# Optimization experiments

Measured on AMD Instinct MI355X. Metric: run time of the kernel, lower is better.

The kernel has to match this reference:

```python
import jax, jax.numpy as jnp
import numpy as np

N = 100000   # nodes
E = 1600000  # edges (nnz of sparse A)
H = 128      # hidden_size


def _row_normalize(x):
    # F.normalize(x, p=1, dim=1): divide each row by max(L1 norm, 1e-12); zero-out infs
    norm = jnp.sum(jnp.abs(x), axis=1, keepdims=True)
    y = x / jnp.maximum(norm, 1e-12)
    return jnp.where(jnp.isinf(y), 0.0, y)


def setup_inputs() -> dict:
    key = jax.random.key(0)
    k = jax.random.split(key, 7)
    x = jax.random.normal(k[0], (N, H), dtype=jnp.float32)
    A_rows = jax.random.randint(k[1], (E,), 0, N, dtype=jnp.int32)
    A_cols = jax.random.randint(k[2], (E,), 0, N, dtype=jnp.int32)
    A_vals = jax.random.uniform(k[3], (E,), dtype=jnp.float32)
    W = jax.random.normal(k[4], (H, H), dtype=jnp.float32) / np.float32(np.sqrt(H))
    b = jax.random.normal(k[5], (H,), dtype=jnp.float32) * 0.01
    time_step = jax.random.uniform(k[6], (1,), dtype=jnp.float32)
    return {"x": x, "A_rows": A_rows, "A_cols": A_cols, "A_vals": A_vals,
            "W": W, "b": b, "time_step": time_step}


def reference(x, A_rows, A_cols, A_vals, W, b, time_step):
    shortcut = x
    xn = _row_normalize(x)                       # normalize=True
    # sparse.mm(A, x): gather neighbor rows, scale by edge value, scatter-add to dst rows
    msgs = A_vals[:, None] * xn[A_cols]          # [E, H]
    f = jax.ops.segment_sum(msgs, A_rows, num_segments=N)  # [N, H]
    f = f @ W.T + b                              # time_varying=True linear
    # dropout p=0 -> identity (eval semantics)
    f = _row_normalize(f)                        # normalize=True
    f = jnp.maximum(f, 0.0)                      # relu
    return shortcut + f * time_step[0]           # Euler residual with learned step
```

## Files before the change

kernel.cpp:

```cpp
#include <hip/hip_runtime.h>

constexpr int HD = 128;
constexpr int BROWS = 64;
constexpr int CAP = 2048;
constexpr int NBMAX = 2048;
constexpr int EPB = 16384;
constexpr int SLOT_STRIDE = 4096;
constexpr int SLOT_BYTES = 32768;

typedef __attribute__((ext_vector_type(8))) short short8v;
typedef __attribute__((ext_vector_type(4))) float f32x4;
typedef __attribute__((ext_vector_type(2))) float f32x2;

__device__ __forceinline__ int rl(int v, int j) {
    return __builtin_amdgcn_readlane(v, j);
}
__device__ __forceinline__ float rlf(int v, int j) {
    return __uint_as_float((unsigned)__builtin_amdgcn_readlane(v, j));
}
__device__ __forceinline__ unsigned f2bf(float f) {
    unsigned u = __float_as_uint(f);
    return (u + 0x7fffu + ((u >> 16) & 1u)) >> 16;
}
__device__ __forceinline__ f32x2 bf2f(unsigned u) {
    f32x2 r = {__uint_as_float(u << 16), __uint_as_float(u & 0xffff0000u)};
    return r;
}

#define META_OFF_MASK 0x03FFFF00

__global__ void init_kernel(int* __restrict__ cursor, int NB) {
    int i = blockIdx.x * 1024 + threadIdx.x;
    if (i < NB) cursor[i] = 0;
}

__global__ void __launch_bounds__(512) build_kernel(
    const float* __restrict__ x, unsigned* __restrict__ xb,
    float* __restrict__ xnorm, const float* __restrict__ W,
    unsigned* __restrict__ Wb, const int* __restrict__ rows,
    const int* __restrict__ cols, const float* __restrict__ vals,
    int* __restrict__ cursor, int2* __restrict__ outslots,
    int2* __restrict__ lastslot, int N, int E, int PB, int NB) {
    int bid = blockIdx.x;
    int tid = threadIdx.x;
    if (bid < PB) {
        int row = bid * 8 + (tid >> 6);
        int lane = tid & 63;
        if (row >= N) return;
        float2 v = *((const float2*)(x + (size_t)row * HD) + lane);
        float s = fabsf(v.x) + fabsf(v.y);
#pragma unroll
        for (int m = 1; m < 64; m <<= 1) s += __shfl_xor(s, m, 64);
        float nm = fmaxf(s, 1e-12f);
        float rn = 1.0f / nm;
        if (lane == 0) xnorm[row] = nm;
        unsigned lo = f2bf(v.x * rn), hi = f2bf(v.y * rn);
        xb[(size_t)row * 64 + lane] = lo | (hi << 16);
    } else if (bid < PB + 16) {
        int t = (bid - PB) * 512 + tid;
        int col = t >> 6, k2 = t & 63;
        float w0 = W[col * HD + 2 * k2];
        float w1 = W[col * HD + 2 * k2 + 1];
        unsigned pk = f2bf(w0) | (f2bf(w1) << 16);
        int byte = (col * 256 + k2 * 4) ^ ((col & 7) << 4);
        *(unsigned*)((char*)Wb + byte) = pk;
    } else {
        int sb = bid - PB - 16;
        if (NB <= NBMAX) {
            __shared__ int lbin[NBMAX];
            __shared__ int lbase[NBMAX];
            __shared__ unsigned short rk16[EPB];
            for (int i = tid; i < NBMAX; i += 512) lbin[i] = 0;
            __syncthreads();
            const int4* rows4 = (const int4*)rows;
            int E4 = E >> 2;
            int base4 = sb * (EPB / 4);
#pragma unroll
            for (int i = 0; i < 8; ++i) {
                int e4 = base4 + i * 512 + tid;
                if (e4 < E4) {
                    int4 r = rows4[e4];
                    int li = (i * 512 + tid) * 4;
                    rk16[li + 0] = (unsigned short)atomicAdd(&lbin[r.x >> 6], 1);
                    rk16[li + 1] = (unsigned short)atomicAdd(&lbin[r.y >> 6], 1);
                    rk16[li + 2] = (unsigned short)atomicAdd(&lbin[r.z >> 6], 1);
                    rk16[li + 3] = (unsigned short)atomicAdd(&lbin[r.w >> 6], 1);
                }
            }
            __syncthreads();
            for (int i = tid; i < NB; i += 512) {
                int c = lbin[i];
                if (c) lbase[i] = atomicAdd(&cursor[i], c);
            }
            __syncthreads();
            const int4* cols4 = (const int4*)cols;
            const float4* vals4 = (const float4*)vals;
#pragma unroll
            for (int i = 0; i < 8; ++i) {
                int e4 = base4 + i * 512 + tid;
                if (e4 < E4) {
                    int4 r4 = rows4[e4];
                    int4 c4 = cols4[e4];
                    float4 v4 = vals4[e4];
                    int li = (i * 512 + tid) * 4;
                    int ra[4] = {r4.x, r4.y, r4.z, r4.w};
                    int ca[4] = {c4.x, c4.y, c4.z, c4.w};
                    float va[4] = {v4.x, v4.y, v4.z, v4.w};
#pragma unroll
                    for (int k = 0; k < 4; ++k) {
                        int r = ra[k];
                        int bkt = r >> 6;
                        int idx = lbase[bkt] + rk16[li + k];
                        if (idx < CAP) {
                            int2* sp = (bkt == NB - 1)
                                           ? lastslot
                                           : outslots + (size_t)bkt * SLOT_STRIDE;
                            sp[idx] = make_int2((ca[k] << 8) | ((r & 63) << 26),
                                                __float_as_int(va[k]));
                        }
                    }
                }
            }
            if (sb == 0) {
                for (int e = (E & ~3) + tid; e < E; e += 512) {
                    int r = rows[e];
                    int bkt = r >> 6;
                    int rel = atomicAdd(&cursor[bkt], 1);
                    if (rel < CAP) {
                        int2* sp = (bkt == NB - 1)
                                       ? lastslot
                                       : outslots + (size_t)bkt * SLOT_STRIDE;
                        sp[rel] = make_int2((cols[e] << 8) | ((r & 63) << 26),
                                            __float_as_int(vals[e]));
                    }
                }
            }
        } else {
            int base = sb * EPB;
            for (int i = 0; i < 32; ++i) {
                int e = base + i * 512 + tid;
                if (e >= E) break;
                int r = rows[e];
                int bkt = r >> 6;
                int rel = atomicAdd(&cursor[bkt], 1);
                if (rel < CAP) {
                    int2* sp = (bkt == NB - 1)
                                   ? lastslot
                                   : outslots + (size_t)bkt * SLOT_STRIDE;
                    sp[rel] = make_int2((cols[e] << 8) | ((r & 63) << 26),
                                        __float_as_int(vals[e]));
                }
            }
        }
    }
}

__global__ void __launch_bounds__(1024) mega_kernel(
    const unsigned* __restrict__ xb, const float* __restrict__ xnorm,
    const int* __restrict__ cursor, const int2* __restrict__ lastslot,
    const unsigned* __restrict__ Wb, const float* __restrict__ bias,
    const float* __restrict__ tsp, float* out, int N, int NB) {
    __shared__ char wb_raw[HD * HD * 2];
    __shared__ char fb_raw[BROWS * HD * 2];
    __shared__ int2 sorted[CAP];
    __shared__ int lcnt[BROWS], lbeg[BROWS], lcur[BROWS];
    __shared__ float rowsum[BROWS];

    int tid = threadIdx.x;
    int bid = blockIdx.x;
    const int2* slot = (bid == NB - 1)
                           ? lastslot
                           : (const int2*)((const char*)out +
                                           (size_t)bid * SLOT_BYTES);
    int ct = cursor[bid];
    if (ct > CAP) ct = CAP;

    if (tid < BROWS) lcnt[tid] = 0;

    int2 m0 = make_int2(0, 0), m1 = make_int2(0, 0);
    bool e0 = tid < ct, e1 = tid + 1024 < ct;
    if (e0) m0 = slot[tid];
    if (e1) m1 = slot[tid + 1024];
    __syncthreads();

    if (e0) atomicAdd(&lcnt[(unsigned)m0.x >> 26], 1);
    if (e1) atomicAdd(&lcnt[(unsigned)m1.x >> 26], 1);
    __syncthreads();

    if (tid < 64) {
        int c = lcnt[tid];
        int s = c;
#pragma unroll
        for (int m = 1; m < 64; m <<= 1) {
            int t2 = __shfl_up(s, m, 64);
            if (tid >= m) s += t2;
        }
        lbeg[tid] = s - c;
        lcur[tid] = s - c;
    }
    __syncthreads();

    if (e0) {
        int p = atomicAdd(&lcur[(unsigned)m0.x >> 26], 1);
        if (p < CAP) sorted[p] = m0;
    }
    if (e1) {
        int p = atomicAdd(&lcur[(unsigned)m1.x >> 26], 1);
        if (p < CAP) sorted[p] = m1;
    }
    {
        const float4* s4 = (const float4*)Wb;
        float4* d4 = (float4*)wb_raw;
        for (int i = tid; i < HD * HD * 2 / 16; i += 1024) d4[i] = s4[i];
    }
    __syncthreads();

    int lane = tid & 63;
    int wid = tid >> 6;
    float ts = tsp[0];
    const char* xbl = (const char*)xb + (lane << 2);

    float a0[4], a1[4];
#pragma unroll
    for (int rr = 0; rr < 4; ++rr) {
        int lr = wid * 4 + rr;
        int beg = lbeg[lr], cnt = lcnt[lr];
        f32x2 pq0 = {0.f, 0.f}, pq1 = {0.f, 0.f};
        for (int jb = 0; jb < cnt; jb += 64) {
            int rem = cnt - jb;
            if (rem > 64) rem = 64;
            int2 meta = make_int2(0, 0);
            if (lane < rem) meta = sorted[beg + jb + lane];
            int j = 0;
            for (; j + 4 <= rem; j += 4) {
                int o0 = rl(meta.x, j) & META_OFF_MASK;
                int o1 = rl(meta.x, j + 1) & META_OFF_MASK;
                int o2 = rl(meta.x, j + 2) & META_OFF_MASK;
                int o3 = rl(meta.x, j + 3) & META_OFF_MASK;
                float s0 = rlf(meta.y, j), s1 = rlf(meta.y, j + 1);
                float s2 = rlf(meta.y, j + 2), s3 = rlf(meta.y, j + 3);
                unsigned u0 = *(const unsigned*)(xbl + o0);
                unsigned u1 = *(const unsigned*)(xbl + o1);
                unsigned u2 = *(const unsigned*)(xbl + o2);
                unsigned u3 = *(const unsigned*)(xbl + o3);
                pq0 += bf2f(u0) * s0;
                pq1 += bf2f(u1) * s1;
                pq0 += bf2f(u2) * s2;
                pq1 += bf2f(u3) * s3;
            }
            for (; j < rem; ++j) {
                int o0 = rl(meta.x, j) & META_OFF_MASK;
                float s0 = rlf(meta.y, j);
                unsigned u0 = *(const unsigned*)(xbl + o0);
                pq0 += bf2f(u0) * s0;
            }
        }
        a0[rr] = pq0.x + pq1.x;
        a1[rr] = pq0.y + pq1.y;
    }

#pragma unroll
    for (int rr = 0; rr < 4; ++rr) {
        int row = wid * 4 + rr;
        unsigned pk = f2bf(a0[rr]) | (f2bf(a1[rr]) << 16);
        int byte = (row * 256 + lane * 4) ^ ((row & 7) << 4);
        *(unsigned*)(fb_raw + byte) = pk;
    }
    if (tid < BROWS) rowsum[tid] = 0.f;
    __syncthreads();

    int rt = wid >> 2;
    int ct0 = (wid & 3) * 2;
    int c = lane & 15;
    int kg = lane >> 4;
    int arow = rt * 16 + c;
    int bcol0 = ct0 * 16 + c;
    int bcol1 = bcol0 + 16;
    f32x4 acc0 = {0.f, 0.f, 0.f, 0.f}, acc1 = {0.f, 0.f, 0.f, 0.f};
#pragma unroll
    for (int kk = 0; kk < 4; ++kk) {
        int ka = kg * 16 + kk * 64;
        short8v af = *(const short8v*)(fb_raw +
                                       ((arow * 256 + ka) ^ ((arow & 7) << 4)));
        short8v bf0 = *(const short8v*)(wb_raw +
                                        ((bcol0 * 256 + ka) ^ ((bcol0 & 7) << 4)));
        short8v bf1 = *(const short8v*)(wb_raw +
                                        ((bcol1 * 256 + ka) ^ ((bcol1 & 7) << 4)));
        acc0 = __builtin_amdgcn_mfma_f32_16x16x32_bf16(af, bf0, acc0, 0, 0, 0);
        acc1 = __builtin_amdgcn_mfma_f32_16x16x32_bf16(af, bf1, acc1, 0, 0, 0);
    }

    float bias0 = bias[bcol0];
    float bias1 = bias[bcol1];
    float g0r[4], g1r[4];
#pragma unroll
    for (int r = 0; r < 4; ++r) {
        float v0 = acc0[r] + bias0;
        float v1 = acc1[r] + bias1;
        g0r[r] = v0;
        g1r[r] = v1;
        float s = fabsf(v0) + fabsf(v1);
        s += __shfl_xor(s, 1, 64);
        s += __shfl_xor(s, 2, 64);
        s += __shfl_xor(s, 4, 64);
        s += __shfl_xor(s, 8, 64);
        if (c == 0) atomicAdd(&rowsum[rt * 16 + kg * 4 + r], s);
    }
    __syncthreads();
#pragma unroll
    for (int r = 0; r < 4; ++r) {
        int lrow = rt * 16 + kg * 4 + r;
        int row = bid * BROWS + lrow;
        if (row < N) {
            float rn = 1.0f / fmaxf(rowsum[lrow], 1e-12f);
            float G0 = fmaxf(g0r[r] * rn, 0.f);
            float G1 = fmaxf(g1r[r] * rn, 0.f);
            float nm = xnorm[row];
            unsigned u0 = xb[(size_t)row * 64 + ct0 * 8 + (c >> 1)];
            unsigned u1 = xb[(size_t)row * 64 + ct0 * 8 + 8 + (c >> 1)];
            unsigned h0 = (c & 1) ? (u0 & 0xffff0000u) : (u0 << 16);
            unsigned h1 = (c & 1) ? (u1 & 0xffff0000u) : (u1 << 16);
            float x0 = __uint_as_float(h0) * nm;
            float x1 = __uint_as_float(h1) * nm;
            out[(size_t)row * HD + bcol0] = fmaf(ts, G0, x0);
            out[(size_t)row * HD + bcol1] = fmaf(ts, G1, x1);
        }
    }
}

extern "C" void kernel_launch(void* const* d_in, const int* in_sizes, int n_in,
                              void* d_out, int out_size, void* d_ws,
                              size_t ws_size, hipStream_t stream) {
    const float* x = (const float*)d_in[0];
    const int* Ar = (const int*)d_in[1];
    const int* Ac = (const int*)d_in[2];
    const float* Av = (const float*)d_in[3];
    const float* W = (const float*)d_in[4];
    const float* b = (const float*)d_in[5];
    const float* ts = (const float*)d_in[6];

    int N = in_sizes[0] / HD;
    int E = in_sizes[1];
    float* out = (float*)d_out;

    int NB = (N + BROWS - 1) / BROWS;

    char* ws = (char*)d_ws;
    size_t o = 0;
    auto take = [&](size_t bytes) {
        void* p = ws + o;
        o += (bytes + 511) & ~(size_t)511;
        return p;
    };
    int* cursor = (int*)take((size_t)NB * 4);
    float* xnorm = (float*)take((size_t)N * 4);
    unsigned* Wb = (unsigned*)take((size_t)HD * HD * 2);
    int2* lastslot = (int2*)take((size_t)CAP * 8);
    unsigned* xb = (unsigned*)take((size_t)N * 64 * 4);

    int PB = (N + 7) / 8;
    int SB = (E + EPB - 1) / EPB;

    init_kernel<<<(NB + 1023) / 1024, 1024, 0, stream>>>(cursor, NB);
    build_kernel<<<PB + 16 + SB, 512, 0, stream>>>(
        x, xb, xnorm, W, Wb, Ar, Ac, Av, cursor, (int2*)d_out, lastslot, N, E,
        PB, NB);
    mega_kernel<<<NB, 1024, 0, stream>>>(xb, xnorm, cursor, lastslot, Wb, b, ts,
                                         out, N, NB);
}
```

Measured before the change: 157.2 us.

## Split build into light prep kernel and separate LDS-heavy scatter kernel

The combined build kernel used about 50KB of shared memory for every block, including the many row-normalize blocks that need none, which limits occupancy. The change moves x normalization, W packing and cursor zeroing into a 256-thread prep kernel with no LDS, and keeps the edge bucketing in its own scatter kernel. This also removes the separate init kernel, so the launch count stays the same. The cost is that prep and scatter no longer overlap within one launch.

```diff
diff --git a/kernel.cpp b/kernel.cpp
--- a/kernel.cpp
+++ b/kernel.cpp
@@ -29,22 +29,17 @@
 
 #define META_OFF_MASK 0x03FFFF00
 
-__global__ void init_kernel(int* __restrict__ cursor, int NB) {
-    int i = blockIdx.x * 1024 + threadIdx.x;
-    if (i < NB) cursor[i] = 0;
-}
-
-__global__ void __launch_bounds__(512) build_kernel(
-    const float* __restrict__ x, unsigned* __restrict__ xb,
-    float* __restrict__ xnorm, const float* __restrict__ W,
-    unsigned* __restrict__ Wb, const int* __restrict__ rows,
-    const int* __restrict__ cols, const float* __restrict__ vals,
-    int* __restrict__ cursor, int2* __restrict__ outslots,
-    int2* __restrict__ lastslot, int N, int E, int PB, int NB) {
+__global__ void prep_kernel(const float* __restrict__ x,
+                            unsigned* __restrict__ xb,
+                            float* __restrict__ xnorm,
+                            const float* __restrict__ W,
+                            unsigned* __restrict__ Wb,
+                            int* __restrict__ cursor,
+                            int N, int PB, int NB) {
     int bid = blockIdx.x;
     int tid = threadIdx.x;
     if (bid < PB) {
-        int row = bid * 8 + (tid >> 6);
+        int row = bid * 4 + (tid >> 6);
         int lane = tid & 63;
         if (row >= N) return;
         float2 v = *((const float2*)(x + (size_t)row * HD) + lane);
@@ -56,8 +51,8 @@
         if (lane == 0) xnorm[row] = nm;
         unsigned lo = f2bf(v.x * rn), hi = f2bf(v.y * rn);
         xb[(size_t)row * 64 + lane] = lo | (hi << 16);
-    } else if (bid < PB + 16) {
-        int t = (bid - PB) * 512 + tid;
+    } else if (bid < PB + 32) {
+        int t = (bid - PB) * 256 + tid;
         int col = t >> 6, k2 = t & 63;
         float w0 = W[col * HD + 2 * k2];
         float w1 = W[col * HD + 2 * k2 + 1];
@@ -65,81 +60,72 @@
         int byte = (col * 256 + k2 * 4) ^ ((col & 7) << 4);
         *(unsigned*)((char*)Wb + byte) = pk;
     } else {
-        int sb = bid - PB - 16;
-        if (NB <= NBMAX) {
-            __shared__ int lbin[NBMAX];
-            __shared__ int lbase[NBMAX];
-            __shared__ unsigned short rk16[EPB];
-            for (int i = tid; i < NBMAX; i += 512) lbin[i] = 0;
-            __syncthreads();
-            const int4* rows4 = (const int4*)rows;
-            int E4 = E >> 2;
-            int base4 = sb * (EPB / 4);
-#pragma unroll
-            for (int i = 0; i < 8; ++i) {
-                int e4 = base4 + i * 512 + tid;
-                if (e4 < E4) {
-                    int4 r = rows4[e4];
-                    int li = (i * 512 + tid) * 4;
-                    rk16[li + 0] = (unsigned short)atomicAdd(&lbin[r.x >> 6], 1);
-                    rk16[li + 1] = (unsigned short)atomicAdd(&lbin[r.y >> 6], 1);
-                    rk16[li + 2] = (unsigned short)atomicAdd(&lbin[r.z >> 6], 1);
-                    rk16[li + 3] = (unsigned short)atomicAdd(&lbin[r.w >> 6], 1);
-                }
-            }
-            __syncthreads();
-            for (int i = tid; i < NB; i += 512) {
-                int c = lbin[i];
-                if (c) lbase[i] = atomicAdd(&cursor[i], c);
-            }
-            __syncthreads();
-            const int4* cols4 = (const int4*)cols;
-            const float4* vals4 = (const float4*)vals;
-#pragma unroll
-            for (int i = 0; i < 8; ++i) {
-                int e4 = base4 + i * 512 + tid;
-                if (e4 < E4) {
-                    int4 r4 = rows4[e4];
-                    int4 c4 = cols4[e4];
-                    float4 v4 = vals4[e4];
-                    int li = (i * 512 + tid) * 4;
-                    int ra[4] = {r4.x, r4.y, r4.z, r4.w};
-                    int ca[4] = {c4.x, c4.y, c4.z, c4.w};
-                    float va[4] = {v4.x, v4.y, v4.z, v4.w};
-#pragma unroll
-                    for (int k = 0; k < 4; ++k) {
-                        int r = ra[k];
-                        int bkt = r >> 6;
-                        int idx = lbase[bkt] + rk16[li + k];
-                        if (idx < CAP) {
-                            int2* sp = (bkt == NB - 1)
-                                           ? lastslot
-                                           : outslots + (size_t)bkt * SLOT_STRIDE;
-                            sp[idx] = make_int2((ca[k] << 8) | ((r & 63) << 26),
-                                                __float_as_int(va[k]));
-                        }
-                    }
-                }
-            }
-            if (sb == 0) {
-                for (int e = (E & ~3) + tid; e < E; e += 512) {
-                    int r = rows[e];
+        for (int i = tid; i < NB; i += 256) cursor[i] = 0;
+    }
+}
+
+__global__ void __launch_bounds__(512) scatter_kernel(
+    const int* __restrict__ rows, const int* __restrict__ cols,
+    const float* __restrict__ vals, int* __restrict__ cursor,
+    int2* __restrict__ outslots, int2* __restrict__ lastslot, int E, int NB) {
+    int tid = threadIdx.x;
+    if (NB <= NBMAX) {
+        __shared__ int lbin[NBMAX];
+        __shared__ int lbase[NBMAX];
+        __shared__ unsigned short rk16[EPB];
+        for (int i = tid; i < NBMAX; i += 512) lbin[i] = 0;
+        __syncthreads();
+        const int4* rows4 = (const int4*)rows;
+        int E4 = E >> 2;
+        int base4 = blockIdx.x * (EPB / 4);
+#pragma unroll
+        for (int i = 0; i < 8; ++i) {
+            int e4 = base4 + i * 512 + tid;
+            if (e4 < E4) {
+                int4 r = rows4[e4];
+                int li = (i * 512 + tid) * 4;
+                rk16[li + 0] = (unsigned short)atomicAdd(&lbin[r.x >> 6], 1);
+                rk16[li + 1] = (unsigned short)atomicAdd(&lbin[r.y >> 6], 1);
+                rk16[li + 2] = (unsigned short)atomicAdd(&lbin[r.z >> 6], 1);
+                rk16[li + 3] = (unsigned short)atomicAdd(&lbin[r.w >> 6], 1);
+            }
+        }
+        __syncthreads();
+        for (int i = tid; i < NB; i += 512) {
+            int c = lbin[i];
+            if (c) lbase[i] = atomicAdd(&cursor[i], c);
+        }
+        __syncthreads();
+        const int4* cols4 = (const int4*)cols;
+        const float4* vals4 = (const float4*)vals;
+#pragma unroll
+        for (int i = 0; i < 8; ++i) {
+            int e4 = base4 + i * 512 + tid;
+            if (e4 < E4) {
+                int4 r4 = rows4[e4];
+                int4 c4 = cols4[e4];
+                float4 v4 = vals4[e4];
+                int li = (i * 512 + tid) * 4;
+                int ra[4] = {r4.x, r4.y, r4.z, r4.w};
+                int ca[4] = {c4.x, c4.y, c4.z, c4.w};
+                float va[4] = {v4.x, v4.y, v4.z, v4.w};
+#pragma unroll
+                for (int k = 0; k < 4; ++k) {
+                    int r = ra[k];
                     int bkt = r >> 6;
-                    int rel = atomicAdd(&cursor[bkt], 1);
-                    if (rel < CAP) {
+                    int idx = lbase[bkt] + rk16[li + k];
+                    if (idx < CAP) {
                         int2* sp = (bkt == NB - 1)
                                        ? lastslot
                                        : outslots + (size_t)bkt * SLOT_STRIDE;
-                        sp[rel] = make_int2((cols[e] << 8) | ((r & 63) << 26),
-                                            __float_as_int(vals[e]));
+                        sp[idx] = make_int2((ca[k] << 8) | ((r & 63) << 26),
+                                            __float_as_int(va[k]));
                     }
                 }
             }
-        } else {
-            int base = sb * EPB;
-            for (int i = 0; i < 32; ++i) {
-                int e = base + i * 512 + tid;
-                if (e >= E) break;
+        }
+        if (blockIdx.x == 0) {
+            for (int e = (E & ~3) + tid; e < E; e += 512) {
                 int r = rows[e];
                 int bkt = r >> 6;
                 int rel = atomicAdd(&cursor[bkt], 1);
@@ -150,6 +136,22 @@
                     sp[rel] = make_int2((cols[e] << 8) | ((r & 63) << 26),
                                         __float_as_int(vals[e]));
                 }
+            }
+        }
+    } else {
+        int base = blockIdx.x * EPB;
+        for (int i = 0; i < 32; ++i) {
+            int e = base + i * 512 + tid;
+            if (e >= E) break;
+            int r = rows[e];
+            int bkt = r >> 6;
+            int rel = atomicAdd(&cursor[bkt], 1);
+            if (rel < CAP) {
+                int2* sp = (bkt == NB - 1)
+                               ? lastslot
+                               : outslots + (size_t)bkt * SLOT_STRIDE;
+                sp[rel] = make_int2((cols[e] << 8) | ((r & 63) << 26),
+                                    __float_as_int(vals[e]));
             }
         }
     }
@@ -358,13 +360,13 @@
     int2* lastslot = (int2*)take((size_t)CAP * 8);
     unsigned* xb = (unsigned*)take((size_t)N * 64 * 4);
 
-    int PB = (N + 7) / 8;
+    int PB = (N + 3) / 4;
     int SB = (E + EPB - 1) / EPB;
 
-    init_kernel<<<(NB + 1023) / 1024, 1024, 0, stream>>>(cursor, NB);
-    build_kernel<<<PB + 16 + SB, 512, 0, stream>>>(
-        x, xb, xnorm, W, Wb, Ar, Ac, Av, cursor, (int2*)d_out, lastslot, N, E,
-        PB, NB);
+    prep_kernel<<<PB + 33, 256, 0, stream>>>(x, xb, xnorm, W, Wb, cursor, N, PB,
+                                             NB);
+    scatter_kernel<<<SB, 512, 0, stream>>>(Ar, Ac, Av, cursor, (int2*)d_out,
+                                           lastslot, E, NB);
     mega_kernel<<<NB, 1024, 0, stream>>>(xb, xnorm, cursor, lastslot, Wb, b, ts,
                                          out, N, NB);
 }
```

Result: faster. 133.0 us (-15.4%).
